# Optimization experiments

Measured on AMD Instinct MI355X. Metric: run time of the kernel, lower is better.

The kernel has to match this reference:

```python
import jax, jax.numpy as jnp
import numpy as np

H = 256          # hidden_dim
D = 64           # dim_dynamic
R = 49           # pooler_resolution ** 2
N = 2000         # bs * num_proposals
EPS = 1e-5


def _ln(x, g, b):
    m = jnp.mean(x, axis=-1, keepdims=True)
    v = jnp.mean(jnp.square(x - m), axis=-1, keepdims=True)
    return (x - m) * jax.lax.rsqrt(v + EPS) * g + b


def setup_inputs() -> dict:
    key = jax.random.key(0)
    ks = jax.random.split(key, 6)
    pro_features = jax.random.normal(ks[0], (1, N, H), dtype=jnp.float32)
    roi_features = jax.random.normal(ks[1], (R, N, H), dtype=jnp.float32)
    # dynamic_layer: Linear(H, num_dynamic * H * D) with num_dynamic = 2
    W_dyn = jax.random.normal(ks[2], (H, 2 * H * D), dtype=jnp.float32) * 0.02
    b_dyn = jnp.zeros((2 * H * D,), dtype=jnp.float32)
    # out_layer: Linear(H * R, H)
    W_out = jax.random.normal(ks[3], (H * R, H), dtype=jnp.float32) * 0.02
    b_out = jnp.zeros((H,), dtype=jnp.float32)
    g1 = jnp.ones((D,), dtype=jnp.float32); b1 = jnp.zeros((D,), dtype=jnp.float32)
    g2 = jnp.ones((H,), dtype=jnp.float32); b2 = jnp.zeros((H,), dtype=jnp.float32)
    g3 = jnp.ones((H,), dtype=jnp.float32); b3 = jnp.zeros((H,), dtype=jnp.float32)
    return {"pro_features": pro_features, "roi_features": roi_features,
            "W_dyn": W_dyn, "b_dyn": b_dyn, "W_out": W_out, "b_out": b_out,
            "g1": g1, "b1": b1, "g2": g2, "b2": b2, "g3": g3, "b3": b3}


def reference(pro_features, roi_features, W_dyn, b_dyn, W_out, b_out,
              g1, b1, g2, b2, g3, b3):
    # roi_features: (R, N, H) -> features: (N, R, H)
    feats = jnp.transpose(roi_features, (1, 0, 2))
    # per-instance dynamic parameters: (N, 2*H*D)
    params = pro_features[0] @ W_dyn + b_dyn
    num_params = H * D
    p1 = params[:, :num_params].reshape(-1, H, D)   # (N, H, D)
    p2 = params[:, num_params:].reshape(-1, D, H)   # (N, D, H)
    f = jnp.einsum('nrh,nhd->nrd', feats, p1)       # bmm 1
    f = jax.nn.relu(_ln(f, g1, b1))
    f = jnp.einsum('nrd,ndh->nrh', f, p2)           # bmm 2
    f = jax.nn.relu(_ln(f, g2, b2))
    f = f.reshape(f.shape[0], R * H)                # flatten(1)
    f = jax.nn.relu(_ln(f @ W_out + b_out, g3, b3))
    return f  # (N, H)
```

## Files before the change

### kernel.cpp

```cpp
#include <hip/hip_runtime.h>

typedef unsigned short u16;
typedef __attribute__((ext_vector_type(8))) short short8;
typedef __attribute__((ext_vector_type(4))) float f32x4;

#define N_INST 2000
#define H_DIM 256
#define D_DIM 64
#define R_DIM 49
#define LN_EPS 1e-5f
#define SPLITK 14

__device__ __forceinline__ u16 f2bf(float f) {
  union { float f; unsigned int i; } x; x.f = f;
  unsigned int r = x.i + 0x7fffu + ((x.i >> 16) & 1u);
  return (u16)(r >> 16);
}
__device__ __forceinline__ float bf2f(u16 u) {
  union { unsigned int i; float f; } x; x.i = ((unsigned int)u) << 16; return x.f;
}
__device__ __forceinline__ short8 ld8(const u16* p) {
  return *reinterpret_cast<const short8*>(p);
}
__device__ __forceinline__ short8 ld8f(const float* p) {
  const float4* q = (const float4*)p;
  float4 a = q[0], b = q[1];
  short8 r;
  r[0] = (short)f2bf(a.x); r[1] = (short)f2bf(a.y);
  r[2] = (short)f2bf(a.z); r[3] = (short)f2bf(a.w);
  r[4] = (short)f2bf(b.x); r[5] = (short)f2bf(b.y);
  r[6] = (short)f2bf(b.z); r[7] = (short)f2bf(b.w);
  return r;
}
__device__ __forceinline__ f32x4 mfma16(short8 a, short8 b, f32x4 c) {
  return __builtin_amdgcn_mfma_f32_16x16x32_bf16(a, b, c, 0, 0, 0);
}
__device__ __forceinline__ void wave_reduce2(float& s, float& s2) {
#pragma unroll
  for (int off = 32; off > 0; off >>= 1) {
    s  += __shfl_down(s, off);
    s2 += __shfl_down(s2, off);
  }
  s = __shfl(s, 0); s2 = __shfl(s2, 0);
}
__device__ __forceinline__ void gload16(const u16* g, u16* l) {
  __builtin_amdgcn_global_load_lds(
      (const __attribute__((address_space(1))) void*)g,
      (__attribute__((address_space(3))) void*)l, 16, 0, 0);
}

__global__ __launch_bounds__(256) void cast_pro(const float* __restrict__ in,
                                                u16* __restrict__ out, int n4) {
  for (int i = blockIdx.x * 256 + threadIdx.x; i < n4; i += gridDim.x * 256) {
    float4 v = ((const float4*)in)[i];
    u16* op = out + i * 4;
    op[0] = f2bf(v.x); op[1] = f2bf(v.y); op[2] = f2bf(v.z); op[3] = f2bf(v.w);
  }
}

__global__ __launch_bounds__(256) void cast_wdyn(const float* __restrict__ W,
                                                 u16* __restrict__ WT, int half) {
  __shared__ u16 T[64][65];
  const int tid = threadIdx.x;
  const int wave = tid >> 6, lane = tid & 63;
  const int b = blockIdx.x;
  const int kt = b >> 8;
  long colbase, rowbase; int rstride;
  if (half == 0) {
    int h = b & 255;
    colbase = (long)h * 64; rowbase = h; rstride = 256;
  } else {
    int d = b & 63, hc = (b >> 6) & 3;
    colbase = 16384L + d * 256 + hc * 64;
    rowbase = 16384L + hc * 4096 + d; rstride = 64;
  }
#pragma unroll
  for (int i = 0; i < 16; ++i) {
    int kk = wave * 16 + i;
    int k = kt * 64 + kk;
    T[kk][lane] = f2bf(W[(long)k * 32768 + colbase + lane]);
  }
  __syncthreads();
#pragma unroll
  for (int i = 0; i < 16; ++i) {
    int jj = wave * 16 + i;
    long ro = rowbase + (long)jj * rstride;
    WT[ro * 256 + kt * 64 + lane] = T[lane][jj];
  }
}

__global__ __launch_bounds__(256) void cast_wout(const float* __restrict__ W,
                                                 u16* __restrict__ WT) {
  __shared__ u16 T[64][65];
  const int tid = threadIdx.x;
  const int wave = tid >> 6, lane = tid & 63;
  const int kt = blockIdx.x >> 2, ct = blockIdx.x & 3;
#pragma unroll
  for (int i = 0; i < 16; ++i) {
    int kk = wave * 16 + i;
    long k = (long)kt * 64 + kk;
    T[kk][lane] = f2bf(W[k * 256 + ct * 64 + lane]);
  }
  __syncthreads();
#pragma unroll
  for (int i = 0; i < 16; ++i) {
    int cc = wave * 16 + i;
    long c = (long)ct * 64 + cc;
    WT[c * 12544 + (long)kt * 64 + lane] = T[lane][cc];
  }
}

__global__ __launch_bounds__(256, 3) void gemm128(
    const u16* __restrict__ A, int lda, int M,
    const u16* __restrict__ BT, int ldbt,
    const float* __restrict__ bias, int bias_mode,
    void* __restrict__ Cout, int ldc, long c_stride_s,
    int ksteps, int n_blocks, int out_f32)
{
  union Smem {
    struct { u16 a[128 * 32]; u16 b[128 * 32]; } s;
    u16 cb[128 * 128];
  };
  __shared__ Smem sm;

  const int tid = threadIdx.x;
  const int wave = tid >> 6, lane = tid & 63;
  const int quad = lane >> 4, l16 = lane & 15;
  const int wm = wave >> 1, wn = wave & 1;
  const int bid = blockIdx.x;
  const int mblk = bid / n_blocks, nblk = bid - mblk * n_blocks;
  const int m0 = mblk * 128, n0 = nblk * 128;
  const int s = blockIdx.y;
  const int kb = s * ksteps * 32;

  const int cl = tid & 3;
  const int r0 = tid >> 2, r1 = 64 + (tid >> 2);
  const int cg0 = cl ^ ((r0 >> 1) & 3);
  const int cg1 = cl ^ ((r1 >> 1) & 3);
  int ga0 = m0 + r0; if (ga0 >= M) ga0 = M - 1;
  int ga1 = m0 + r1; if (ga1 >= M) ga1 = M - 1;
  const u16* gA0 = A + (long)ga0 * lda + kb + cg0 * 8;
  const u16* gA1 = A + (long)ga1 * lda + kb + cg1 * 8;
  const u16* gB0 = BT + (long)(n0 + r0) * ldbt + kb + cg0 * 8;
  const u16* gB1 = BT + (long)(n0 + r1) * ldbt + kb + cg1 * 8;
  u16* lA0 = &sm.s.a[tid * 8];
  u16* lA1 = &sm.s.a[(tid + 256) * 8];
  u16* lB0 = &sm.s.b[tid * 8];
  u16* lB1 = &sm.s.b[(tid + 256) * 8];

  const u16* fA[4]; const u16* fB[4];
#pragma unroll
  for (int i = 0; i < 4; ++i) {
    int rt = wm * 64 + i * 16 + l16;
    fA[i] = &sm.s.a[rt * 32 + (quad ^ ((rt >> 1) & 3)) * 8];
    int ct = wn * 64 + i * 16 + l16;
    fB[i] = &sm.s.b[ct * 32 + (quad ^ ((ct >> 1) & 3)) * 8];
  }

  f32x4 acc[4][4];
#pragma unroll
  for (int mi = 0; mi < 4; ++mi)
#pragma unroll
    for (int ni = 0; ni < 4; ++ni) acc[mi][ni] = f32x4{0.f, 0.f, 0.f, 0.f};

  for (int ks = 0; ks < ksteps; ++ks) {
    const int ko = ks * 32;
    gload16(gA0 + ko, lA0);
    gload16(gA1 + ko, lA1);
    gload16(gB0 + ko, lB0);
    gload16(gB1 + ko, lB1);
    __syncthreads();
    short8 av[4], bv[4];
#pragma unroll
    for (int i = 0; i < 4; ++i) { av[i] = ld8(fA[i]); bv[i] = ld8(fB[i]); }
#pragma unroll
    for (int mi = 0; mi < 4; ++mi)
#pragma unroll
      for (int ni = 0; ni < 4; ++ni)
        acc[mi][ni] = mfma16(av[mi], bv[ni], acc[mi][ni]);
    __syncthreads();
  }

  if (!out_f32) {
    float bvv[4];
#pragma unroll
    for (int ni = 0; ni < 4; ++ni) {
      int col = n0 + wn * 64 + ni * 16 + l16;
      int bi = col;
      if (bias_mode == 1)      bi = ((col & 255) << 6) + (col >> 8);
      else if (bias_mode == 2) bi = 16384 + ((col & 63) << 8) + (col >> 6);
      bvv[ni] = bias ? bias[bi] : 0.f;
    }
#pragma unroll
    for (int mi = 0; mi < 4; ++mi)
#pragma unroll
      for (int ni = 0; ni < 4; ++ni)
#pragma unroll
        for (int i = 0; i < 4; ++i) {
          int row = wm * 64 + mi * 16 + quad * 4 + i;
          int col = wn * 64 + ni * 16 + l16;
          sm.cb[row * 128 + col] = f2bf(acc[mi][ni][i] + bvv[ni]);
        }
    __syncthreads();
    u16* Cp = (u16*)Cout;
#pragma unroll
    for (int j = 0; j < 8; ++j) {
      int lin = j * 2048 + tid * 8;
      int row = lin >> 7, col = lin & 127;
      int grow = m0 + row;
      if (grow < M)
        *reinterpret_cast<short8*>(Cp + (long)grow * ldc + n0 + col) =
            ld8(&sm.cb[lin]);
    }
  } else {
    float* Cp = (float*)Cout + (long)s * c_stride_s;
#pragma unroll
    for (int mi = 0; mi < 4; ++mi)
#pragma unroll
      for (int ni = 0; ni < 4; ++ni) {
        int col = n0 + wn * 64 + ni * 16 + l16;
#pragma unroll
        for (int i = 0; i < 4; ++i) {
          int row = m0 + wm * 64 + mi * 16 + quad * 4 + i;
          if (row < M) Cp[(long)row * ldc + col] = acc[mi][ni][i];
        }
      }
  }
}

__global__ __launch_bounds__(256) void bmm1_ln(
    const float* __restrict__ roi,
    const u16* __restrict__ P1T,
    const float* __restrict__ g1, const float* __restrict__ b1,
    u16* __restrict__ f1n)
{
  const int n = blockIdx.x;
  const int tid = threadIdx.x;
  const int wave = tid >> 6, lane = tid & 63;
  const int quad = lane >> 4, l16 = lane & 15;

  union SmemU {
    u16 bt[D_DIM][H_DIM + 8];
    float cb[64][D_DIM];
  };
  __shared__ SmemU sm;

  const u16* P1n = P1T + (long)n * (H_DIM * D_DIM);
#pragma unroll
  for (int i = 0; i < 8; ++i) {
    int idx = (tid + 256 * i) * 8;
    int d = idx >> 8, hg = idx & 255;
    *reinterpret_cast<short8*>(&sm.bt[d][hg]) = ld8(P1n + idx);
  }
  __syncthreads();

  int r = wave * 16 + l16;
  int rr = (r < R_DIM) ? r : 0;
  const float* Arow = roi + ((long)rr * N_INST + n) * H_DIM + quad * 8;

  f32x4 acc[4];
#pragma unroll
  for (int i = 0; i < 4; ++i) acc[i] = f32x4{0.f, 0.f, 0.f, 0.f};

#pragma unroll
  for (int ks = 0; ks < 8; ++ks) {
    short8 af = ld8f(Arow + ks * 32);
#pragma unroll
    for (int sub = 0; sub < 4; ++sub) {
      short8 bf = ld8(&sm.bt[sub * 16 + l16][ks * 32 + quad * 8]);
      acc[sub] = mfma16(af, bf, acc[sub]);
    }
  }
  __syncthreads();
#pragma unroll
  for (int sub = 0; sub < 4; ++sub)
#pragma unroll
    for (int i = 0; i < 4; ++i)
      sm.cb[wave * 16 + quad * 4 + i][sub * 16 + l16] = acc[sub][i];
  __syncthreads();

  float gv = g1[lane], bv = b1[lane];
  for (int i = 0; i < 13; ++i) {
    int r2 = wave + 4 * i;
    if (r2 < R_DIM) {
      float x = sm.cb[r2][lane];
      float sv = x, s2 = x * x;
      wave_reduce2(sv, s2);
      float mean = sv * (1.f / 64.f);
      float var = s2 * (1.f / 64.f) - mean * mean;
      float rs = rsqrtf(var + LN_EPS);
      float y = fmaxf((x - mean) * rs * gv + bv, 0.f);
      f1n[((long)n * R_DIM + r2) * D_DIM + lane] = f2bf(y);
    }
  }
}

__global__ __launch_bounds__(256) void bmm2_ln(
    const u16* __restrict__ f1n,
    const u16* __restrict__ P2T,
    const float* __restrict__ g2, const float* __restrict__ b2,
    u16* __restrict__ f2n)
{
  const int n = blockIdx.x;
  const int tid = threadIdx.x;
  const int wave = tid >> 6, lane = tid & 63;
  const int quad = lane >> 4, l16 = lane & 15;

  union SmemU {
    u16 bt[H_DIM][D_DIM + 8];
    u16 cb[R_DIM][H_DIM];
  };
  __shared__ SmemU sm;

  const u16* P2n = P2T + (long)n * (D_DIM * H_DIM);
#pragma unroll
  for (int i = 0; i < 8; ++i) {
    int idx = (tid + 256 * i) * 8;
    int h = idx >> 6, dg = idx & 63;
    *reinterpret_cast<short8*>(&sm.bt[h][dg]) = ld8(P2n + idx);
  }
  __syncthreads();

  int r = wave * 16 + l16;
  int rr = (r < R_DIM) ? r : 0;
  const u16* Arow = f1n + ((long)n * R_DIM + rr) * D_DIM + quad * 8;

  f32x4 acc[16];
#pragma unroll
  for (int i = 0; i < 16; ++i) acc[i] = f32x4{0.f, 0.f, 0.f, 0.f};

#pragma unroll
  for (int ks = 0; ks < 2; ++ks) {
    short8 af = ld8(Arow + ks * 32);
#pragma unroll
    for (int sub = 0; sub < 16; ++sub) {
      short8 bf = ld8(&sm.bt[sub * 16 + l16][ks * 32 + quad * 8]);
      acc[sub] = mfma16(af, bf, acc[sub]);
    }
  }
  __syncthreads();
#pragma unroll
  for (int sub = 0; sub < 16; ++sub)
#pragma unroll
    for (int i = 0; i < 4; ++i) {
      int row = wave * 16 + quad * 4 + i;
      if (row < R_DIM) sm.cb[row][sub * 16 + l16] = f2bf(acc[sub][i]);
    }
  __syncthreads();

  float4 gv = *(const float4*)&g2[lane * 4];
  float4 bv = *(const float4*)&b2[lane * 4];
  for (int i = 0; i < 13; ++i) {
    int r2 = wave + 4 * i;
    if (r2 < R_DIM) {
      ushort4 xv = *reinterpret_cast<const ushort4*>(&sm.cb[r2][lane * 4]);
      float x0 = bf2f(xv.x), x1 = bf2f(xv.y), x2 = bf2f(xv.z), x3 = bf2f(xv.w);
      float sv = x0 + x1 + x2 + x3;
      float s2 = x0 * x0 + x1 * x1 + x2 * x2 + x3 * x3;
      wave_reduce2(sv, s2);
      float mean = sv * (1.f / 256.f);
      float var = s2 * (1.f / 256.f) - mean * mean;
      float rs = rsqrtf(var + LN_EPS);
      ushort4 yv;
      yv.x = f2bf(fmaxf((x0 - mean) * rs * gv.x + bv.x, 0.f));
      yv.y = f2bf(fmaxf((x1 - mean) * rs * gv.y + bv.y, 0.f));
      yv.z = f2bf(fmaxf((x2 - mean) * rs * gv.z + bv.z, 0.f));
      yv.w = f2bf(fmaxf((x3 - mean) * rs * gv.w + bv.w, 0.f));
      *reinterpret_cast<ushort4*>(
          &f2n[((long)n * R_DIM + r2) * H_DIM + lane * 4]) = yv;
    }
  }
}

__global__ __launch_bounds__(64) void ln3_k(
    const float* __restrict__ partial,
    const float* __restrict__ b_out,
    const float* __restrict__ g3, const float* __restrict__ b3,
    float* __restrict__ out)
{
  const int n = blockIdx.x;
  const int lane = threadIdx.x;
  float x[4], sv = 0.f, s2 = 0.f;
#pragma unroll
  for (int j = 0; j < 4; ++j) {
    int h = lane + 64 * j;
    float v = b_out[h];
#pragma unroll
    for (int ss = 0; ss < SPLITK; ++ss)
      v += partial[((long)ss * N_INST + n) * H_DIM + h];
    x[j] = v; sv += v; s2 += v * v;
  }
  wave_reduce2(sv, s2);
  float mean = sv * (1.f / 256.f);
  float var = s2 * (1.f / 256.f) - mean * mean;
  float rs = rsqrtf(var + LN_EPS);
#pragma unroll
  for (int j = 0; j < 4; ++j) {
    int h = lane + 64 * j;
    float y = fmaxf((x[j] - mean) * rs * g3[h] + b3[h], 0.f);
    out[(long)n * H_DIM + h] = y;
  }
}

extern "C" void kernel_launch(void* const* d_in, const int* in_sizes, int n_in,
                              void* d_out, int out_size, void* d_ws, size_t ws_size,
                              hipStream_t stream) {
  const float* pro  = (const float*)d_in[0];
  const float* roi  = (const float*)d_in[1];
  const float* Wdyn = (const float*)d_in[2];
  const float* bdyn = (const float*)d_in[3];
  const float* Wout = (const float*)d_in[4];
  const float* bout = (const float*)d_in[5];
  const float* g1 = (const float*)d_in[6];
  const float* b1 = (const float*)d_in[7];
  const float* g2 = (const float*)d_in[8];
  const float* b2 = (const float*)d_in[9];
  const float* g3 = (const float*)d_in[10];
  const float* b3 = (const float*)d_in[11];
  float* out = (float*)d_out;

  char* ws = (char*)d_ws;
  u16* proB   = (u16*)ws;
  u16* WdynT  = (u16*)(ws + 1024000);
  u16* WoutT  = (u16*)(ws + 17801216);
  u16* params = (u16*)(ws + 24223744);
  u16* f1n    = (u16*)(ws + 89759744);
  u16* f2n    = (u16*)(ws + 102303744);
  float* partial = (float*)(ws + 24223744);

  dim3 blk(256);
  const int HD = H_DIM * D_DIM;

  cast_pro<<<dim3(500), blk, 0, stream>>>(pro, proB, 512000 / 4);
  cast_wdyn<<<dim3(1024), blk, 0, stream>>>(Wdyn, WdynT, 0);
  cast_wdyn<<<dim3(1024), blk, 0, stream>>>(Wdyn, WdynT, 1);
  cast_wout<<<dim3(784), blk, 0, stream>>>(Wout, WoutT);

  gemm128<<<dim3(16 * 128, 1), blk, 0, stream>>>(
      proB, H_DIM, N_INST, WdynT, H_DIM, bdyn, 1,
      (void*)params, HD, 0L, 8, 128, 0);
  bmm1_ln<<<dim3(N_INST), blk, 0, stream>>>(roi, params, g1, b1, f1n);
  gemm128<<<dim3(16 * 128, 1), blk, 0, stream>>>(
      proB, H_DIM, N_INST, WdynT + (long)16384 * 256, H_DIM, bdyn, 2,
      (void*)params, HD, 0L, 8, 128, 0);
  bmm2_ln<<<dim3(N_INST), blk, 0, stream>>>(f1n, params, g2, b2, f2n);
  gemm128<<<dim3(16 * 2, SPLITK), blk, 0, stream>>>(
      f2n, R_DIM * H_DIM, N_INST, WoutT, R_DIM * H_DIM, nullptr, 0,
      (void*)partial, H_DIM, (long)N_INST * H_DIM, 28, 2, 1);
  ln3_k<<<dim3(N_INST), dim3(64), 0, stream>>>(partial, bout, g3, b3, out);
}
```

Baseline: 358.1 us.

## Double-buffer GEMM LDS tiles and use async swizzled LDS loads in bmm kernels

The tiled GEMM now keeps two LDS buffers, so the next k-step's global-to-LDS loads are issued before the current tile's MFMAs, and one barrier per iteration is removed. The bmm1 and bmm2 kernels issue their activation row loads into registers first, then fill LDS with the per-instance parameter matrix through direct global-to-LDS loads using an XOR swizzle instead of padding, overlapping the two loads. Costs are double the GEMM LDS footprint, which may lower occupancy, and more register pressure from the preloaded rows in bmm1.

Measured after the change: 345.6 us. -3.5%, faster.

```diff
diff --git a/kernel.cpp b/kernel.cpp
--- a/kernel.cpp
+++ b/kernel.cpp
@@ -22,9 +22,7 @@
 __device__ __forceinline__ short8 ld8(const u16* p) {
   return *reinterpret_cast<const short8*>(p);
 }
-__device__ __forceinline__ short8 ld8f(const float* p) {
-  const float4* q = (const float4*)p;
-  float4 a = q[0], b = q[1];
+__device__ __forceinline__ short8 pack8(float4 a, float4 b) {
   short8 r;
   r[0] = (short)f2bf(a.x); r[1] = (short)f2bf(a.y);
   r[2] = (short)f2bf(a.z); r[3] = (short)f2bf(a.w);
@@ -118,7 +116,7 @@
     int ksteps, int n_blocks, int out_f32)
 {
   union Smem {
-    struct { u16 a[128 * 32]; u16 b[128 * 32]; } s;
+    struct { u16 a[2][128 * 32]; u16 b[2][128 * 32]; } s;
     u16 cb[128 * 128];
   };
   __shared__ Smem sm;
@@ -143,18 +141,14 @@
   const u16* gA1 = A + (long)ga1 * lda + kb + cg1 * 8;
   const u16* gB0 = BT + (long)(n0 + r0) * ldbt + kb + cg0 * 8;
   const u16* gB1 = BT + (long)(n0 + r1) * ldbt + kb + cg1 * 8;
-  u16* lA0 = &sm.s.a[tid * 8];
-  u16* lA1 = &sm.s.a[(tid + 256) * 8];
-  u16* lB0 = &sm.s.b[tid * 8];
-  u16* lB1 = &sm.s.b[(tid + 256) * 8];
-
-  const u16* fA[4]; const u16* fB[4];
+
+  int fAoff[4], fBoff[4];
 #pragma unroll
   for (int i = 0; i < 4; ++i) {
     int rt = wm * 64 + i * 16 + l16;
-    fA[i] = &sm.s.a[rt * 32 + (quad ^ ((rt >> 1) & 3)) * 8];
+    fAoff[i] = rt * 32 + (quad ^ ((rt >> 1) & 3)) * 8;
     int ct = wn * 64 + i * 16 + l16;
-    fB[i] = &sm.s.b[ct * 32 + (quad ^ ((ct >> 1) & 3)) * 8];
+    fBoff[i] = ct * 32 + (quad ^ ((ct >> 1) & 3)) * 8;
   }
 
   f32x4 acc[4][4];
@@ -163,22 +157,32 @@
 #pragma unroll
     for (int ni = 0; ni < 4; ++ni) acc[mi][ni] = f32x4{0.f, 0.f, 0.f, 0.f};
 
+  gload16(gA0, &sm.s.a[0][tid * 8]);
+  gload16(gA1, &sm.s.a[0][(tid + 256) * 8]);
+  gload16(gB0, &sm.s.b[0][tid * 8]);
+  gload16(gB1, &sm.s.b[0][(tid + 256) * 8]);
+
   for (int ks = 0; ks < ksteps; ++ks) {
-    const int ko = ks * 32;
-    gload16(gA0 + ko, lA0);
-    gload16(gA1 + ko, lA1);
-    gload16(gB0 + ko, lB0);
-    gload16(gB1 + ko, lB1);
+    const int cur = ks & 1, nxt = cur ^ 1;
     __syncthreads();
+    if (ks + 1 < ksteps) {
+      const int ko = (ks + 1) * 32;
+      gload16(gA0 + ko, &sm.s.a[nxt][tid * 8]);
+      gload16(gA1 + ko, &sm.s.a[nxt][(tid + 256) * 8]);
+      gload16(gB0 + ko, &sm.s.b[nxt][tid * 8]);
+      gload16(gB1 + ko, &sm.s.b[nxt][(tid + 256) * 8]);
+    }
     short8 av[4], bv[4];
 #pragma unroll
-    for (int i = 0; i < 4; ++i) { av[i] = ld8(fA[i]); bv[i] = ld8(fB[i]); }
+    for (int i = 0; i < 4; ++i) {
+      av[i] = ld8(&sm.s.a[cur][fAoff[i]]);
+      bv[i] = ld8(&sm.s.b[cur][fBoff[i]]);
+    }
 #pragma unroll
     for (int mi = 0; mi < 4; ++mi)
 #pragma unroll
       for (int ni = 0; ni < 4; ++ni)
         acc[mi][ni] = mfma16(av[mi], bv[ni], acc[mi][ni]);
-    __syncthreads();
   }
 
   if (!out_f32) {
@@ -191,6 +195,7 @@
       else if (bias_mode == 2) bi = 16384 + ((col & 63) << 8) + (col >> 6);
       bvv[ni] = bias ? bias[bi] : 0.f;
     }
+    __syncthreads();
 #pragma unroll
     for (int mi = 0; mi < 4; ++mi)
 #pragma unroll
@@ -240,23 +245,30 @@
   const int quad = lane >> 4, l16 = lane & 15;
 
   union SmemU {
-    u16 bt[D_DIM][H_DIM + 8];
+    u16 bt[D_DIM * H_DIM];
     float cb[64][D_DIM];
   };
   __shared__ SmemU sm;
 
-  const u16* P1n = P1T + (long)n * (H_DIM * D_DIM);
-#pragma unroll
-  for (int i = 0; i < 8; ++i) {
-    int idx = (tid + 256 * i) * 8;
-    int d = idx >> 8, hg = idx & 255;
-    *reinterpret_cast<short8*>(&sm.bt[d][hg]) = ld8(P1n + idx);
-  }
-  __syncthreads();
-
   int r = wave * 16 + l16;
   int rr = (r < R_DIM) ? r : 0;
   const float* Arow = roi + ((long)rr * N_INST + n) * H_DIM + quad * 8;
+  float4 rv[16];
+#pragma unroll
+  for (int ks = 0; ks < 8; ++ks) {
+    rv[2 * ks]     = ((const float4*)(Arow + ks * 32))[0];
+    rv[2 * ks + 1] = ((const float4*)(Arow + ks * 32))[1];
+  }
+
+  const u16* P1n = P1T + (long)n * (H_DIM * D_DIM);
+#pragma unroll
+  for (int j = 0; j < 8; ++j) {
+    int lc = j * 256 + tid;
+    int d = lc >> 5, c = lc & 31;
+    int cg = (c & 24) | ((c & 7) ^ (d & 7));
+    gload16(P1n + d * 256 + cg * 8, &sm.bt[lc * 8]);
+  }
+  __syncthreads();
 
   f32x4 acc[4];
 #pragma unroll
@@ -264,10 +276,13 @@
 
 #pragma unroll
   for (int ks = 0; ks < 8; ++ks) {
-    short8 af = ld8f(Arow + ks * 32);
+    short8 af = pack8(rv[2 * ks], rv[2 * ks + 1]);
 #pragma unroll
     for (int sub = 0; sub < 4; ++sub) {
-      short8 bf = ld8(&sm.bt[sub * 16 + l16][ks * 32 + quad * 8]);
+      int d = sub * 16 + l16;
+      int q = ks * 4 + quad;
+      int c = (q & 24) | ((q & 7) ^ (d & 7));
+      short8 bf = ld8(&sm.bt[d * 256 + c * 8]);
       acc[sub] = mfma16(af, bf, acc[sub]);
     }
   }
@@ -307,23 +322,26 @@
   const int quad = lane >> 4, l16 = lane & 15;
 
   union SmemU {
-    u16 bt[H_DIM][D_DIM + 8];
+    u16 bt[H_DIM * D_DIM];
     u16 cb[R_DIM][H_DIM];
   };
   __shared__ SmemU sm;
 
-  const u16* P2n = P2T + (long)n * (D_DIM * H_DIM);
-#pragma unroll
-  for (int i = 0; i < 8; ++i) {
-    int idx = (tid + 256 * i) * 8;
-    int h = idx >> 6, dg = idx & 63;
-    *reinterpret_cast<short8*>(&sm.bt[h][dg]) = ld8(P2n + idx);
-  }
-  __syncthreads();
-
   int r = wave * 16 + l16;
   int rr = (r < R_DIM) ? r : 0;
   const u16* Arow = f1n + ((long)n * R_DIM + rr) * D_DIM + quad * 8;
+  short8 af0 = ld8(Arow);
+  short8 af1 = ld8(Arow + 32);
+
+  const u16* P2n = P2T + (long)n * (D_DIM * H_DIM);
+#pragma unroll
+  for (int j = 0; j < 8; ++j) {
+    int lc = j * 256 + tid;
+    int h = lc >> 3, c = lc & 7;
+    int cg = c ^ (h & 7);
+    gload16(P2n + h * 64 + cg * 8, &sm.bt[lc * 8]);
+  }
+  __syncthreads();
 
   f32x4 acc[16];
 #pragma unroll
@@ -331,10 +349,12 @@
 
 #pragma unroll
   for (int ks = 0; ks < 2; ++ks) {
-    short8 af = ld8(Arow + ks * 32);
+    short8 af = ks ? af1 : af0;
 #pragma unroll
     for (int sub = 0; sub < 16; ++sub) {
-      short8 bf = ld8(&sm.bt[sub * 16 + l16][ks * 32 + quad * 8]);
+      int h = sub * 16 + l16;
+      int c = (ks * 4 + quad) ^ (h & 7);
+      short8 bf = ld8(&sm.bt[h * 64 + c * 8]);
       acc[sub] = mfma16(af, bf, acc[sub]);
     }
   }
```
